# Kernel optimization log

Measured on AMD Instinct MI355X. Metric: run time of the kernel, lower is better.

## Reference

```python
import jax, jax.numpy as jnp
import numpy as np

N = 10000   # nodes
K = 8       # out-degree per node (uniform)
E = N * K   # edges
D = 64      # d_embed (also per-head dim: projection is d_embed -> d_embed*n_heads)
H = 8       # n_heads
DE = 16     # d_e_embed (also per-edge-head dim)
EH = 4      # e_heads
EPS = 1e-16


def seg_softmax(src, index, num):
    # torch_geometric.utils.softmax: per-segment max-subtract, exp, normalize
    mx = jax.ops.segment_max(src, index, num_segments=num)
    mx = jnp.where(jnp.isfinite(mx), mx, 0.0)
    ex = jnp.exp(src - mx[index])
    s = jax.ops.segment_sum(ex, index, num_segments=num)
    return ex / (s[index] + EPS)


def _lin(k, out_d, in_d):
    # xavier-uniform-ish weight, zero bias (matches init_weights)
    bound = float(np.sqrt(6.0 / (in_d + out_d)))
    W = jax.random.uniform(k, (out_d, in_d), jnp.float32, -bound, bound)
    return W, jnp.zeros((out_d,), jnp.float32)


def setup_inputs() -> dict:
    key = jax.random.key(0)
    ks = jax.random.split(key, 12)
    x = jax.random.normal(ks[0], (N, D), jnp.float32)
    row0 = jnp.repeat(jnp.arange(N, dtype=jnp.int32), K)          # sorted sources
    row1 = jax.random.randint(ks[1], (E,), 0, N, jnp.int32)        # random targets
    edge_index = jnp.stack([row0, row1])                           # [2, E]
    # n^3 pair indices (uniform degree => closed form matching torch helper)
    eiq = jnp.repeat(jnp.arange(E, dtype=jnp.int32), K)            # repeat_interleave within node block
    eik = jnp.broadcast_to(jnp.arange(E, dtype=jnp.int32).reshape(N, 1, K), (N, K, K)).reshape(-1)  # tile within block
    edge_features = jax.random.normal(ks[2], (E, DE), jnp.float32)
    Wq, bq = _lin(ks[3], D * H, D)
    Wk, bk = _lin(ks[4], D * H, D)
    Wv, bv = _lin(ks[5], D * H, D)
    Wlin, blin = _lin(ks[6], D, H * D)
    Weq, beq = _lin(ks[7], DE * EH, DE)
    Wev, bev = _lin(ks[8], DE * EH, DE)
    Wek, bek = _lin(ks[9], DE * EH, H)
    Wel, bel = _lin(ks[10], H, EH * DE)
    Wele, bele = _lin(ks[11], DE, H)
    return dict(x=x, edge_features=edge_features,
                Wq=Wq, bq=bq, Wk=Wk, bk=bk, Wv=Wv, bv=bv, Wlin=Wlin, blin=blin,
                Weq=Weq, beq=beq, Wev=Wev, bev=bev, Wek=Wek, bek=bek,
                Wel=Wel, bel=bel, Wele=Wele, bele=bele,
                edge_index=edge_index, eiq=eiq, eik=eik)


def reference(x, edge_features, Wq, bq, Wk, bk, Wv, bv, Wlin, blin,
              Weq, beq, Wev, bev, Wek, bek, Wel, bel, Wele, bele,
              edge_index, eiq, eik):
    e0, e1 = edge_index[0], edge_index[1]
    nq = (x @ Wq.T + bq).reshape(N, H, D)
    nk = (x @ Wk.T + bk).reshape(N, H, D)
    nv = (x @ Wv.T + bv).reshape(N, H, D)
    # per-edge scaled dot product: [E, H]
    sqk = (nq[e0] * nk[e1]).sum(-1) / jnp.sqrt(jnp.float32(D))
    # --- edge attention over edge-edge pairs ---
    eq = (edge_features @ Weq.T + beq).reshape(E, EH, DE)
    ev = (edge_features @ Wev.T + bev).reshape(E, EH, DE)
    ek = (sqk @ Wek.T + bek).reshape(E, EH, DE)
    seqk = (eq[eiq] * ek[eik]).sum(-1) / jnp.sqrt(jnp.float32(DE))   # [P, EH]
    att_e = seg_softmax(seqk, eiq, E)
    eout = jax.ops.segment_sum(att_e[:, :, None] * ev[eik], eiq, num_segments=E)  # [E, EH, DE]
    edge_emb = eout.reshape(E, EH * DE) @ Wel.T + bel                # [E, H]
    # --- node attention with edge-modulated scores ---
    att_n = seg_softmax(edge_emb + sqk, e0, N)                       # [E, H]
    node = jax.ops.segment_sum(att_n[:, :, None] * nv[e1], e0, num_segments=N)    # [N, H, D]
    node_embeddings = node.reshape(N, H * D) @ Wlin.T + blin         # [N, D]
    edge_embeddings = edge_emb @ Wele.T + bele                       # [E, DE]
    return node_embeddings, edge_embeddings
```

## Files before the change

kernel.cpp:

```cpp
#include <hip/hip_runtime.h>

typedef unsigned short u16;
typedef unsigned int   u32;

#define N_NODES 10000
#define N_EDGES 80000

typedef __attribute__((ext_vector_type(8))) short bf16x8;
typedef __attribute__((ext_vector_type(4))) float fx4;
#define MFMA16(a, b, c) __builtin_amdgcn_mfma_f32_16x16x32_bf16(a, b, c, 0, 0, 0)

__device__ __forceinline__ u16 f2bf(float f) {
    union { float f; u32 i; } c; c.f = f;
    u32 u = c.i;
    u32 r = (u + 0x7fffu + ((u >> 16) & 1u)) >> 16;
    return (u16)r;
}
__device__ __forceinline__ float bf2f(u16 u) {
    union { u32 i; float f; } c; c.i = ((u32)u) << 16; return c.f;
}
__device__ __forceinline__ void unpack8(uint4 w, float* v) {
    union { u32 i; float f; } c;
    c.i = w.x << 16; v[0] = c.f; c.i = w.x & 0xffff0000u; v[1] = c.f;
    c.i = w.y << 16; v[2] = c.f; c.i = w.y & 0xffff0000u; v[3] = c.f;
    c.i = w.z << 16; v[4] = c.f; c.i = w.z & 0xffff0000u; v[5] = c.f;
    c.i = w.w << 16; v[6] = c.f; c.i = w.w & 0xffff0000u; v[7] = c.f;
}

__device__ __forceinline__ void wsync() {
    asm volatile("s_waitcnt lgkmcnt(0)" ::: "memory");
    __builtin_amdgcn_wave_barrier();
}


__device__ __forceinline__ void stage_w(const float* src, int rstride,
                                        u16* wh, u16* wl, int t) {
    const int row = t >> 2, seg = t & 3;
    const float* p = src + (long)row * rstride + seg * 16;
    float v[16];
    #pragma unroll
    for (int q = 0; q < 4; ++q) *(float4*)&v[q * 4] = *(const float4*)(p + q * 4);
    u16 hh[16], ll[16];
    #pragma unroll
    for (int j = 0; j < 16; ++j) {
        u16 hi = f2bf(v[j]);
        hh[j] = hi;
        ll[j] = f2bf(v[j] - bf2f(hi));
    }
    const int base = row * 72 + seg * 16;
    *(uint4*)&wh[base]     = *(uint4*)&hh[0];
    *(uint4*)&wh[base + 8] = *(uint4*)&hh[8];
    *(uint4*)&wl[base]     = *(uint4*)&ll[0];
    *(uint4*)&wl[base + 8] = *(uint4*)&ll[8];
}

__device__ __forceinline__ void load_a64(const float* m, int arow, int ko,
                                         bf16x8 ah[2], bf16x8 al[2]) {
    if (arow < N_NODES) {
        #pragma unroll
        for (int ks = 0; ks < 2; ++ks) {
            const float* p = m + (long)arow * 64 + ks * 32 + ko;
            float v[8];
            *(float4*)&v[0] = *(const float4*)p;
            *(float4*)&v[4] = *(const float4*)(p + 4);
            #pragma unroll
            for (int j = 0; j < 8; ++j) {
                u16 hi = f2bf(v[j]);
                ah[ks][j] = (short)hi;
                al[ks][j] = (short)f2bf(v[j] - bf2f(hi));
            }
        }
    } else {
        #pragma unroll
        for (int ks = 0; ks < 2; ++ks) { ah[ks] = (bf16x8)0; al[ks] = (bf16x8)0; }
    }
}

__device__ __forceinline__ fx4 gemm3(const bf16x8 ah[2], const bf16x8 al[2],
                                     const u16* wh, const u16* wl,
                                     int colrow, int ko) {
    fx4 acc = {0.f, 0.f, 0.f, 0.f};
    #pragma unroll
    for (int ks = 0; ks < 2; ++ks) {
        const bf16x8 bh = *(const bf16x8*)&wh[colrow * 72 + ks * 32 + ko];
        const bf16x8 bl = *(const bf16x8*)&wl[colrow * 72 + ks * 32 + ko];
        acc = MFMA16(al[ks], bh, acc);
        acc = MFMA16(ah[ks], bl, acc);
        acc = MFMA16(ah[ks], bh, acc);
    }
    return acc;
}

__global__ __launch_bounds__(256) void proj_kernel(
    const float* __restrict__ x,
    const float* __restrict__ Wq, const float* __restrict__ bq,
    const float* __restrict__ Wk, const float* __restrict__ bk,
    const float* __restrict__ Wv, const float* __restrict__ bv,
    const float* __restrict__ Wlin,
    float* __restrict__ NQ, u16* __restrict__ NK, u16* __restrict__ G)
{
    __shared__ __align__(16) u16 wh[64 * 72];
    __shared__ __align__(16) u16 wl[64 * 72];
    __shared__ __align__(16) u16 nvh[4 * 16 * 72];
    __shared__ __align__(16) u16 nvl[4 * 16 * 72];

    const int t  = threadIdx.x;
    const int l  = t & 63, w = t >> 6;
    const int ko = (l >> 4) * 8;
    const int r0 = blockIdx.x * 64;
    const int h  = blockIdx.y;
    const int c0 = h * 64;

    bf16x8 ah[2], al[2];
    load_a64(x, r0 + w * 16 + (l & 15), ko, ah, al);

    fx4 acc[4];

    stage_w(Wq + (long)c0 * 64, 64, wh, wl, t);
    __syncthreads();
    #pragma unroll
    for (int cf = 0; cf < 4; ++cf)
        acc[cf] = gemm3(ah, al, wh, wl, cf * 16 + (l & 15), ko);
    #pragma unroll
    for (int cf = 0; cf < 4; ++cf) {
        const int col = c0 + cf * 16 + (l & 15);
        const float bias = bq[col];
        #pragma unroll
        for (int j = 0; j < 4; ++j) {
            const int gr = r0 + w * 16 + (l >> 4) * 4 + j;
            if (gr < N_NODES) NQ[(long)gr * 512 + col] = acc[cf][j] + bias;
        }
    }
    __syncthreads();

    stage_w(Wk + (long)c0 * 64, 64, wh, wl, t);
    __syncthreads();
    #pragma unroll
    for (int cf = 0; cf < 4; ++cf)
        acc[cf] = gemm3(ah, al, wh, wl, cf * 16 + (l & 15), ko);
    #pragma unroll
    for (int cf = 0; cf < 4; ++cf) {
        const int col = c0 + cf * 16 + (l & 15);
        const float bias = bk[col];
        #pragma unroll
        for (int j = 0; j < 4; ++j) {
            const int gr = r0 + w * 16 + (l >> 4) * 4 + j;
            if (gr < N_NODES) NK[(long)gr * 512 + col] = f2bf(acc[cf][j] + bias);
        }
    }
    __syncthreads();

    stage_w(Wv + (long)c0 * 64, 64, wh, wl, t);
    __syncthreads();
    #pragma unroll
    for (int cf = 0; cf < 4; ++cf)
        acc[cf] = gemm3(ah, al, wh, wl, cf * 16 + (l & 15), ko);
    #pragma unroll
    for (int cf = 0; cf < 4; ++cf) {
        const int col = cf * 16 + (l & 15);
        const float bias = bv[c0 + col];
        #pragma unroll
        for (int j = 0; j < 4; ++j) {
            const int rloc = (l >> 4) * 4 + j;
            float v = acc[cf][j] + bias;
            u16 hi = f2bf(v);
            nvh[w * 1152 + rloc * 72 + col] = hi;
            nvl[w * 1152 + rloc * 72 + col] = f2bf(v - bf2f(hi));
        }
    }
    __syncthreads();
    stage_w(Wlin + c0, 512, wh, wl, t);
    __syncthreads();

    bf16x8 a2h[2], a2l[2];
    #pragma unroll
    for (int ks = 0; ks < 2; ++ks) {
        a2h[ks] = *(const bf16x8*)&nvh[w * 1152 + (l & 15) * 72 + ks * 32 + ko];
        a2l[ks] = *(const bf16x8*)&nvl[w * 1152 + (l & 15) * 72 + ks * 32 + ko];
    }
    #pragma unroll
    for (int cf = 0; cf < 4; ++cf)
        acc[cf] = gemm3(a2h, a2l, wh, wl, cf * 16 + (l & 15), ko);

    #pragma unroll
    for (int cf = 0; cf < 4; ++cf) {
        const int col = c0 + cf * 16 + (l & 15);
        #pragma unroll
        for (int j = 0; j < 4; ++j) {
            const int gr = r0 + w * 16 + (l >> 4) * 4 + j;
            if (gr < N_NODES) G[(long)gr * 512 + col] = f2bf(acc[cf][j]);
        }
    }
}

#define SLAB_F 2272
__global__ __launch_bounds__(256, 4) void node_kernel(
    const float* __restrict__ ef, const int* __restrict__ e1,
    const float* __restrict__ NQ, const u16* __restrict__ NK,
    const u16* __restrict__ G,
    const float* __restrict__ Weq, const float* __restrict__ beq,
    const float* __restrict__ Wev, const float* __restrict__ bev,
    const float* __restrict__ Wek, const float* __restrict__ bek,
    const float* __restrict__ Wel, const float* __restrict__ bel,
    const float* __restrict__ Wele, const float* __restrict__ bele,
    const float* __restrict__ blin,
    float* __restrict__ out_node, float* __restrict__ out_edge)
{
    __shared__ __align__(16) float well[8 * 68];
    __shared__ __align__(16) float slabs[4][SLAB_F];

    const int t   = threadIdx.x;
    const int t64 = t & 63;
    const int wv  = t >> 6;
    const int n   = (int)__builtin_amdgcn_readfirstlane(blockIdx.x * 4 + wv);

    float* S      = slabs[wv];
    float* eqb    = S;
    float* ekb    = S + 544;
    float* evb    = S + 1088;
    float* eob    = eqb;
    float* sl     = S + 1632;
    float* efl    = S + 1920;
    u16*   gbuf   = (u16*)S;
    float* sqk_l  = S + 2080;
    float* emb_l  = S + 2144;
    float* attn_l = S + 2208;

    int tg[8];
    #pragma unroll
    for (int i = 0; i < 8; ++i) tg[i] = e1[n * 8 + i];

    float q8[8];
    {
        const float4* p = (const float4*)(NQ + (long)n * 512 + t64 * 8);
        *(float4*)&q8[0] = p[0];
        *(float4*)&q8[4] = p[1];
    }
    uint4 kreg[8];
    #pragma unroll
    for (int i = 0; i < 8; ++i)
        kreg[i] = *(const uint4*)(NK + (long)tg[i] * 512 + t64 * 8);

    float2 efv = ((const float2*)(ef + (long)n * 128))[t64];

    float wq16[16], wv16[16], wk8[8], wele8[8];
    {
        const float4* p = (const float4*)(Weq + t64 * 16);
        #pragma unroll
        for (int q4 = 0; q4 < 4; ++q4) *(float4*)&wq16[q4 * 4] = p[q4];
        const float4* q = (const float4*)(Wev + t64 * 16);
        #pragma unroll
        for (int q4 = 0; q4 < 4; ++q4) *(float4*)&wv16[q4 * 4] = q[q4];
        const float4* r = (const float4*)(Wek + t64 * 8);
        *(float4*)&wk8[0] = r[0]; *(float4*)&wk8[4] = r[1];
        const float4* s = (const float4*)(Wele + (t64 & 15) * 8);
        *(float4*)&wele8[0] = s[0]; *(float4*)&wele8[4] = s[1];
    }
    const float beqv = beq[t64], bevv = bev[t64], bekv = bek[t64];
    const float bele_t = bele[t64 & 15];
    const float blin_t = blin[t64];

    #pragma unroll
    for (int rep = 0; rep < 2; ++rep) {
        const int idx = rep * 256 + t;
        well[(idx >> 6) * 68 + (idx & 63)] = Wel[idx];
    }
    efl[2 * t64] = efv.x; efl[2 * t64 + 1] = efv.y;

    {
        float part[8];
        #pragma unroll
        for (int i = 0; i < 8; ++i) {
            float kv[8]; unpack8(kreg[i], kv);
            float s = q8[0] * kv[0] + q8[1] * kv[1] + q8[2] * kv[2] + q8[3] * kv[3]
                    + q8[4] * kv[4] + q8[5] * kv[5] + q8[6] * kv[6] + q8[7] * kv[7];
            part[i] = s;
        }
        #pragma unroll
        for (int m = 1; m <= 4; m <<= 1) {
            #pragma unroll
            for (int i = 0; i < 8; ++i) part[i] += __shfl_xor(part[i], m);
        }
        const int h8 = t64 >> 3, dc = t64 & 7;
        sqk_l[dc * 8 + h8] = part[dc] * 0.125f;
    }
    __syncthreads();

    #pragma unroll
    for (int i = 0; i < 8; ++i) {
        float aq = beqv, av = bevv;
        #pragma unroll
        for (int q = 0; q < 4; ++q) {
            float4 f = *(const float4*)&efl[i * 16 + q * 4];
            aq += f.x * wq16[q * 4] + f.y * wq16[q * 4 + 1] + f.z * wq16[q * 4 + 2] + f.w * wq16[q * 4 + 3];
            av += f.x * wv16[q * 4] + f.y * wv16[q * 4 + 1] + f.z * wv16[q * 4 + 2] + f.w * wv16[q * 4 + 3];
        }
        float ak = bekv;
        #pragma unroll
        for (int q = 0; q < 2; ++q) {
            float4 s = *(const float4*)&sqk_l[i * 8 + q * 4];
            ak += s.x * wk8[q * 4] + s.y * wk8[q * 4 + 1] + s.z * wk8[q * 4 + 2] + s.w * wk8[q * 4 + 3];
        }
        eqb[i * 68 + t64] = aq; evb[i * 68 + t64] = av; ekb[i * 68 + t64] = ak;
    }
    wsync();

    {
        const int i = t64 >> 3, j = t64 & 7;
        #pragma unroll
        for (int eh = 0; eh < 4; ++eh) {
            float acc = 0.f;
            #pragma unroll
            for (int q = 0; q < 4; ++q) {
                float4 a = *(const float4*)&eqb[i * 68 + eh * 16 + q * 4];
                float4 b = *(const float4*)&ekb[j * 68 + eh * 16 + q * 4];
                acc += a.x * b.x + a.y * b.y + a.z * b.z + a.w * b.w;
            }
            sl[eh * 72 + i * 8 + j] = acc * 0.25f;
        }
    }
    wsync();

    if (t64 < 32) {
        const int i = t64 >> 2, eh = t64 & 3;
        float4 v0 = *(const float4*)&sl[eh * 72 + i * 8];
        float4 v1 = *(const float4*)&sl[eh * 72 + i * 8 + 4];
        float mx = fmaxf(fmaxf(fmaxf(v0.x, v0.y), fmaxf(v0.z, v0.w)),
                         fmaxf(fmaxf(v1.x, v1.y), fmaxf(v1.z, v1.w)));
        float e0 = __expf(v0.x - mx), e1_ = __expf(v0.y - mx);
        float e2 = __expf(v0.z - mx), e3  = __expf(v0.w - mx);
        float e4 = __expf(v1.x - mx), e5  = __expf(v1.y - mx);
        float e6 = __expf(v1.z - mx), e7  = __expf(v1.w - mx);
        float inv = 1.f / (e0 + e1_ + e2 + e3 + e4 + e5 + e6 + e7 + 1e-16f);
        float4 w0 = {e0 * inv, e1_ * inv, e2 * inv, e3 * inv};
        float4 w1 = {e4 * inv, e5 * inv, e6 * inv, e7 * inv};
        *(float4*)&sl[eh * 72 + i * 8]     = w0;
        *(float4*)&sl[eh * 72 + i * 8 + 4] = w1;
    }
    wsync();

    {
        const int eh = t64 >> 4;
        #pragma unroll
        for (int i = 0; i < 8; ++i) {
            float4 s0 = *(const float4*)&sl[eh * 72 + i * 8];
            float4 s1 = *(const float4*)&sl[eh * 72 + i * 8 + 4];
            float acc = s0.x * evb[0 * 68 + t64] + s0.y * evb[1 * 68 + t64]
                      + s0.z * evb[2 * 68 + t64] + s0.w * evb[3 * 68 + t64]
                      + s1.x * evb[4 * 68 + t64] + s1.y * evb[5 * 68 + t64]
                      + s1.z * evb[6 * 68 + t64] + s1.w * evb[7 * 68 + t64];
            eob[i * 68 + t64] = acc;
        }
    }
    wsync();

    {
        const int i = t64 >> 3, h = t64 & 7;
        float acc = bel[h];
        #pragma unroll
        for (int q = 0; q < 16; ++q) {
            float4 a  = *(const float4*)&eob[i * 68 + q * 4];
            float4 ww = *(const float4*)&well[h * 68 + q * 4];
            acc += a.x * ww.x + a.y * ww.y + a.z * ww.z + a.w * ww.w;
        }
        emb_l[i * 8 + h] = acc;
    }
    wsync();

    uint4 greg[8];
    {
        const int i = t64 >> 3, c8 = t64 & 7;
        const uint4* gp = (const uint4*)(G + (long)tg[i] * 512);
        #pragma unroll
        for (int q = 0; q < 8; ++q) greg[q] = gp[c8 + q * 8];
    }

    #pragma unroll
    for (int rep = 0; rep < 2; ++rep) {
        const int idx = rep * 64 + t64;
        const int i = idx >> 4;
        float acc = bele_t;
        #pragma unroll
        for (int h = 0; h < 8; ++h) acc += emb_l[i * 8 + h] * wele8[h];
        out_edge[(long)n * 128 + idx] = acc;
    }

    if (t64 < 8) {
        const int h = t64;
        float lg[8], mx = -1e30f;
        #pragma unroll
        for (int i = 0; i < 8; ++i) { lg[i] = emb_l[i * 8 + h] + sqk_l[i * 8 + h]; mx = fmaxf(mx, lg[i]); }
        float sum = 0.f;
        #pragma unroll
        for (int i = 0; i < 8; ++i) { float e = __expf(lg[i] - mx); attn_l[i * 8 + h] = e; sum += e; }
        float inv = 1.f / (sum + 1e-16f);
        #pragma unroll
        for (int i = 0; i < 8; ++i) attn_l[i * 8 + h] *= inv;
    }

    {
        const int i = t64 >> 3, c8 = t64 & 7;
        #pragma unroll
        for (int q = 0; q < 8; ++q)
            *(uint4*)&gbuf[i * 520 + (c8 + q * 8) * 8] = greg[q];
    }
    wsync();

    {
        float acc = blin_t;
        #pragma unroll
        for (int i = 0; i < 8; ++i) {
            float4 a0 = *(const float4*)&attn_l[i * 8];
            float4 a1 = *(const float4*)&attn_l[i * 8 + 4];
            const u16* gr = &gbuf[i * 520];
            acc += a0.x * bf2f(gr[0 * 64 + t64]) + a0.y * bf2f(gr[1 * 64 + t64])
                 + a0.z * bf2f(gr[2 * 64 + t64]) + a0.w * bf2f(gr[3 * 64 + t64])
                 + a1.x * bf2f(gr[4 * 64 + t64]) + a1.y * bf2f(gr[5 * 64 + t64])
                 + a1.z * bf2f(gr[6 * 64 + t64]) + a1.w * bf2f(gr[7 * 64 + t64]);
        }
        out_node[(long)n * 64 + t64] = acc;
    }
}

extern "C" void kernel_launch(void* const* d_in, const int* in_sizes, int n_in,
                              void* d_out, int out_size, void* d_ws, size_t ws_size,
                              hipStream_t stream) {
    (void)in_sizes; (void)n_in; (void)out_size; (void)ws_size;
    const float* x    = (const float*)d_in[0];
    const float* ef   = (const float*)d_in[1];
    const float* Wq   = (const float*)d_in[2];
    const float* bq   = (const float*)d_in[3];
    const float* Wk   = (const float*)d_in[4];
    const float* bk   = (const float*)d_in[5];
    const float* Wv   = (const float*)d_in[6];
    const float* bv   = (const float*)d_in[7];
    const float* Wlin = (const float*)d_in[8];
    const float* blin = (const float*)d_in[9];
    const float* Weq  = (const float*)d_in[10];
    const float* beq  = (const float*)d_in[11];
    const float* Wev  = (const float*)d_in[12];
    const float* bev  = (const float*)d_in[13];
    const float* Wek  = (const float*)d_in[14];
    const float* bek  = (const float*)d_in[15];
    const float* Wel  = (const float*)d_in[16];
    const float* bel  = (const float*)d_in[17];
    const float* Wele = (const float*)d_in[18];
    const float* bele = (const float*)d_in[19];
    const int* edge_index = (const int*)d_in[20];
    const int* e1 = edge_index + N_EDGES;

    float* out_node = (float*)d_out;
    float* out_edge = (float*)d_out + 640000;

    char* ws = (char*)d_ws;
    u16*   NK = (u16*)ws;
    u16*   G  = (u16*)(ws + 10240000);
    float* NQ = (float*)(ws + 20480000);

    proj_kernel<<<dim3(157, 8), 256, 0, stream>>>(x, Wq, bq, Wk, bk, Wv, bv, Wlin,
                                                  NQ, NK, G);
    node_kernel<<<2500, 256, 0, stream>>>(ef, e1, NQ, NK, G,
                                          Weq, beq, Wev, bev, Wek, bek,
                                          Wel, bel, Wele, bele, blin,
                                          out_node, out_edge);
}
```

Before: 163.6 us.

## Keep edge values and gathered G rows in registers, shrink LDS slab

Edge value projections stay in registers instead of an LDS buffer. The final node aggregation now reduces gathered G rows directly from registers via cross-lane shuffles instead of staging them through shared memory. The G gather is issued earlier to overlap with the edge-embedding step. These cuts reduce LDS per wave and allow raising launch bounds from 4 to 5 blocks per CU. The risk is more register pressure and extra shuffle work, which could cause spills or offset the occupancy gain.

Result: slower. 227.5 us (+39.0%).

```diff
diff --git a/kernel.cpp b/kernel.cpp
--- a/kernel.cpp
+++ b/kernel.cpp
@@ -193,8 +193,8 @@
     }
 }
 
-#define SLAB_F 2272
-__global__ __launch_bounds__(256, 4) void node_kernel(
+#define SLAB_F 1696
+__global__ __launch_bounds__(256, 5) void node_kernel(
     const float* __restrict__ ef, const int* __restrict__ e1,
     const float* __restrict__ NQ, const u16* __restrict__ NK,
     const u16* __restrict__ G,
@@ -217,14 +217,12 @@
     float* S      = slabs[wv];
     float* eqb    = S;
     float* ekb    = S + 544;
-    float* evb    = S + 1088;
     float* eob    = eqb;
-    float* sl     = S + 1632;
-    float* efl    = S + 1920;
-    u16*   gbuf   = (u16*)S;
-    float* sqk_l  = S + 2080;
-    float* emb_l  = S + 2144;
-    float* attn_l = S + 2208;
+    float* sl     = S + 1088;
+    float* efl    = S + 1376;
+    float* sqk_l  = S + 1504;
+    float* emb_l  = S + 1568;
+    float* attn_l = S + 1632;
 
     int tg[8];
     #pragma unroll
@@ -258,7 +256,7 @@
     }
     const float beqv = beq[t64], bevv = bev[t64], bekv = bek[t64];
     const float bele_t = bele[t64 & 15];
-    const float blin_t = blin[t64];
+    const float blin_c = blin[(t64 & 7) * 8 + (t64 >> 3)];
 
     #pragma unroll
     for (int rep = 0; rep < 2; ++rep) {
@@ -286,6 +284,7 @@
     }
     __syncthreads();
 
+    float ev_reg[8];
     #pragma unroll
     for (int i = 0; i < 8; ++i) {
         float aq = beqv, av = bevv;
@@ -301,7 +300,8 @@
             float4 s = *(const float4*)&sqk_l[i * 8 + q * 4];
             ak += s.x * wk8[q * 4] + s.y * wk8[q * 4 + 1] + s.z * wk8[q * 4 + 2] + s.w * wk8[q * 4 + 3];
         }
-        eqb[i * 68 + t64] = aq; evb[i * 68 + t64] = av; ekb[i * 68 + t64] = ak;
+        eqb[i * 68 + t64] = aq; ekb[i * 68 + t64] = ak;
+        ev_reg[i] = av;
     }
     wsync();
 
@@ -345,14 +345,22 @@
         for (int i = 0; i < 8; ++i) {
             float4 s0 = *(const float4*)&sl[eh * 72 + i * 8];
             float4 s1 = *(const float4*)&sl[eh * 72 + i * 8 + 4];
-            float acc = s0.x * evb[0 * 68 + t64] + s0.y * evb[1 * 68 + t64]
-                      + s0.z * evb[2 * 68 + t64] + s0.w * evb[3 * 68 + t64]
-                      + s1.x * evb[4 * 68 + t64] + s1.y * evb[5 * 68 + t64]
-                      + s1.z * evb[6 * 68 + t64] + s1.w * evb[7 * 68 + t64];
+            float acc = s0.x * ev_reg[0] + s0.y * ev_reg[1]
+                      + s0.z * ev_reg[2] + s0.w * ev_reg[3]
+                      + s1.x * ev_reg[4] + s1.y * ev_reg[5]
+                      + s1.z * ev_reg[6] + s1.w * ev_reg[7];
             eob[i * 68 + t64] = acc;
         }
     }
     wsync();
+
+    uint4 greg[8];
+    {
+        const int i = t64 >> 3, c8 = t64 & 7;
+        const uint4* gp = (const uint4*)(G + (long)tg[i] * 512);
+        #pragma unroll
+        for (int q = 0; q < 8; ++q) greg[q] = gp[c8 + q * 8];
+    }
 
     {
         const int i = t64 >> 3, h = t64 & 7;
@@ -367,14 +375,6 @@
     }
     wsync();
 
-    uint4 greg[8];
-    {
-        const int i = t64 >> 3, c8 = t64 & 7;
-        const uint4* gp = (const uint4*)(G + (long)tg[i] * 512);
-        #pragma unroll
-        for (int q = 0; q < 8; ++q) greg[q] = gp[c8 + q * 8];
-    }
-
     #pragma unroll
     for (int rep = 0; rep < 2; ++rep) {
         const int idx = rep * 64 + t64;
@@ -397,28 +397,31 @@
         #pragma unroll
         for (int i = 0; i < 8; ++i) attn_l[i * 8 + h] *= inv;
     }
-
-    {
-        const int i = t64 >> 3, c8 = t64 & 7;
-        #pragma unroll
-        for (int q = 0; q < 8; ++q)
-            *(uint4*)&gbuf[i * 520 + (c8 + q * 8) * 8] = greg[q];
-    }
-    wsync();
-
-    {
-        float acc = blin_t;
-        #pragma unroll
-        for (int i = 0; i < 8; ++i) {
-            float4 a0 = *(const float4*)&attn_l[i * 8];
-            float4 a1 = *(const float4*)&attn_l[i * 8 + 4];
-            const u16* gr = &gbuf[i * 520];
-            acc += a0.x * bf2f(gr[0 * 64 + t64]) + a0.y * bf2f(gr[1 * 64 + t64])
-                 + a0.z * bf2f(gr[2 * 64 + t64]) + a0.w * bf2f(gr[3 * 64 + t64])
-                 + a1.x * bf2f(gr[4 * 64 + t64]) + a1.y * bf2f(gr[5 * 64 + t64])
-                 + a1.z * bf2f(gr[6 * 64 + t64]) + a1.w * bf2f(gr[7 * 64 + t64]);
-        }
-        out_node[(long)n * 64 + t64] = acc;
+    wsync();
+
+    {
+        const int i = t64 >> 3;
+        float4 a0 = *(const float4*)&attn_l[i * 8];
+        float4 a1 = *(const float4*)&attn_l[i * 8 + 4];
+        const float aq[8] = {a0.x, a0.y, a0.z, a0.w, a1.x, a1.y, a1.z, a1.w};
+        float part[8];
+        #pragma unroll
+        for (int j = 0; j < 8; ++j) part[j] = 0.f;
+        #pragma unroll
+        for (int q = 0; q < 8; ++q) {
+            float gv[8]; unpack8(greg[q], gv);
+            #pragma unroll
+            for (int j = 0; j < 8; ++j) part[j] += aq[q] * gv[j];
+        }
+        #pragma unroll
+        for (int m = 8; m <= 32; m <<= 1) {
+            #pragma unroll
+            for (int j = 0; j < 8; ++j) part[j] += __shfl_xor(part[j], m);
+        }
+        float sel = part[0];
+        #pragma unroll
+        for (int j = 1; j < 8; ++j) sel = (i == j) ? part[j] : sel;
+        out_node[(long)n * 64 + (t64 & 7) * 8 + i] = sel + blin_c;
     }
 }
 
```
